# Kernel tuning notes

Hardware: AMD Instinct MI355X
Metric: run time of the kernel (lower is better)

The kernel has to match this reference:

```python
import jax, jax.numpy as jnp
import numpy as np

B, S, D, H = 4, 1024, 1024, 16
HD = D // H


def setup_inputs() -> dict:
    key = jax.random.key(0)
    ks = jax.random.split(key, 8)
    x = jax.random.normal(ks[0], (B, S, D), dtype=jnp.float32)
    attn_bias = jax.random.normal(ks[1], (B, H, S, S), dtype=jnp.float32) * 0.1
    pos_ids = jnp.broadcast_to(jnp.arange(S, dtype=jnp.int32), (B, S))
    lengths = jnp.array([S, S - 64, S - 128, S - 256], dtype=jnp.int32)
    pad_mask = jnp.arange(S)[None, :] >= lengths[:, None]  # True = padded key
    scale = 0.02
    Wq = jax.random.normal(ks[2], (D, D), dtype=jnp.float32) * scale
    Wk = jax.random.normal(ks[3], (D, D), dtype=jnp.float32) * scale
    Wv = jax.random.normal(ks[4], (D, D), dtype=jnp.float32) * scale
    Wo = jax.random.normal(ks[5], (D, D), dtype=jnp.float32) * scale
    bq = jnp.zeros((D,), jnp.float32); bk = jnp.zeros((D,), jnp.float32)
    bv = jnp.zeros((D,), jnp.float32); bo = jnp.zeros((D,), jnp.float32)
    return {"x": x, "attn_bias": attn_bias, "pos_ids": pos_ids, "pad_mask": pad_mask,
            "Wq": Wq, "bq": bq, "Wk": Wk, "bk": bk, "Wv": Wv, "bv": bv, "Wo": Wo, "bo": bo}


def _apply_rotary(q, k, pos_ids):
    # q,k: [B,S,H,HD]; pos_ids: [B,S]
    hd = q.shape[-1]
    inv_freq = 1.0 / (10000.0 ** (jnp.arange(0, hd, 2, dtype=jnp.float32) / hd))
    freqs = pos_ids.astype(jnp.float32)[:, :, None] * inv_freq  # [B,S,HD/2]
    emb = jnp.concatenate([freqs, freqs], axis=-1)[:, :, None, :]  # [B,S,1,HD]
    cos, sin = jnp.cos(emb), jnp.sin(emb)
    def rot_half(t):
        t1, t2 = jnp.split(t, 2, axis=-1)
        return jnp.concatenate([-t2, t1], axis=-1)
    return q * cos + rot_half(q) * sin, k * cos + rot_half(k) * sin


def reference(x, attn_bias, pos_ids, pad_mask, Wq, bq, Wk, bk, Wv, bv, Wo, bo):
    b, s, d = x.shape
    q = (x @ Wq.T + bq).reshape(b, s, H, HD)
    k = (x @ Wk.T + bk).reshape(b, s, H, HD)
    v = (x @ Wv.T + bv).reshape(b, s, H, HD)
    q, k = _apply_rotary(q, k, pos_ids)
    q = q.transpose(0, 2, 1, 3)  # [B,H,S,HD]
    k = k.transpose(0, 2, 1, 3)
    v = v.transpose(0, 2, 1, 3)
    scores = jnp.einsum("bhqd,bhkd->bhqk", q, k) / np.sqrt(HD).astype(np.float32)
    scores = scores + attn_bias
    scores = jnp.where(pad_mask[:, None, None, :], -jnp.inf, scores)
    attn = jax.nn.softmax(scores, axis=-1)  # dropout p=0 -> identity
    out = jnp.einsum("bhqk,bhkd->bqhd", attn, v).reshape(b, s, d)
    metric = k.mean(axis=1)  # mean over heads -> [B,S,HD]
    return out @ Wo.T + bo, metric
```

## Files before the change

kernel.cpp:

```cpp
#include <hip/hip_runtime.h>
#include <hip/hip_bf16.h>

#define SS 1024
#define DD 1024
#define HH 16
#define HDD 64

using f32x4  = __attribute__((ext_vector_type(4))) float;
using bf16x8 = __attribute__((ext_vector_type(8))) __bf16;
using bf16x4 = __attribute__((ext_vector_type(4))) __bf16;

__device__ __forceinline__ void gload_lds16(const void* g, void* l) {
  __builtin_amdgcn_global_load_lds((__attribute__((address_space(1))) void*)g,
                                   (__attribute__((address_space(3))) void*)l, 16, 0, 0);
}

__global__ void convert_kernel(const float4* __restrict__ x, const float4* __restrict__ Wq,
                               const float4* __restrict__ Wk, const float4* __restrict__ Wv,
                               const float4* __restrict__ Wo,
                               bf16x4* __restrict__ xb, bf16x4* __restrict__ wqkvb,
                               bf16x4* __restrict__ wob, float4* __restrict__ metric) {
  int i = blockIdx.x * 256 + threadIdx.x;
  if (blockIdx.x < 256) {
    float4 z = {0.f, 0.f, 0.f, 0.f};
    metric[blockIdx.x * 256 + threadIdx.x] = z;
  }
  float4 v; bf16x4* dst;
  if (i < 1048576)      { v = x[i];              dst = xb + i; }
  else if (i < 1310720) { v = Wq[i - 1048576];   dst = wqkvb + (i - 1048576); }
  else if (i < 1572864) { v = Wk[i - 1310720];   dst = wqkvb + 262144 + (i - 1310720); }
  else if (i < 1835008) { v = Wv[i - 1572864];   dst = wqkvb + 524288 + (i - 1572864); }
  else                  { v = Wo[i - 1835008];   dst = wob + (i - 1835008); }
  bf16x4 o;
  o[0] = (__bf16)v.x; o[1] = (__bf16)v.y; o[2] = (__bf16)v.z; o[3] = (__bf16)v.w;
  *dst = o;
}

template<int EPI>
__global__ __launch_bounds__(256, 2)
void gemm_kernel(const __bf16* __restrict__ A, const __bf16* __restrict__ Bm, int N,
                 const float* __restrict__ b0, const float* __restrict__ b1,
                 const float* __restrict__ b2, const int* __restrict__ pos_ids,
                 __bf16* __restrict__ Qr, __bf16* __restrict__ Kr, __bf16* __restrict__ Vtg,
                 float* __restrict__ metric, float* __restrict__ Cout) {
  __shared__ __align__(16) char smem[17408];
  __bf16* As = (__bf16*)smem;
  __bf16* Bs = (__bf16*)(smem + 8192);
  const int tid = threadIdx.x;
  const int wid = tid >> 6, lane = tid & 63;
  const int g = lane >> 4, cl = lane & 15;
  const int ntn = N >> 7;
  const int bm = blockIdx.x / ntn, bn = blockIdx.x % ntn;
  const int m0 = bm << 7, n0 = bn << 7;
  const int wr = (wid >> 1) << 6, wc = (wid & 1) << 6;

  f32x4 acc[4][4] = {};

  for (int kk = 0; kk < 1024; kk += 32) {
    __syncthreads();
#pragma unroll
    for (int p = 0; p < 2; ++p) {
      int idx = p * 256 + tid;
      gload_lds16(A  + (size_t)(m0 + (idx >> 2)) * 1024 + kk + ((idx & 3) << 3),
                  (char*)As + p * 4096 + wid * 1024);
      gload_lds16(Bm + (size_t)(n0 + (idx >> 2)) * 1024 + kk + ((idx & 3) << 3),
                  (char*)Bs + p * 4096 + wid * 1024);
    }
    __syncthreads();
    bf16x8 fa[4], fb[4];
#pragma unroll
    for (int i = 0; i < 4; ++i)
      fa[i] = *(const bf16x8*)(As + (wr + i * 16 + cl) * 32 + g * 8);
#pragma unroll
    for (int j = 0; j < 4; ++j)
      fb[j] = *(const bf16x8*)(Bs + (wc + j * 16 + cl) * 32 + g * 8);
#pragma unroll
    for (int i = 0; i < 4; ++i)
#pragma unroll
      for (int j = 0; j < 4; ++j)
        acc[i][j] = __builtin_amdgcn_mfma_f32_16x16x32_bf16(fa[i], fb[j], acc[i][j], 0, 0, 0);
  }

  if constexpr (EPI == 1) {
#pragma unroll
    for (int j = 0; j < 4; ++j) {
      int col = n0 + wc + j * 16 + cl;
      float bv = b0[col];
#pragma unroll
      for (int i = 0; i < 4; ++i)
#pragma unroll
        for (int r = 0; r < 4; ++r) {
          int row = m0 + wr + i * 16 + g * 4 + r;
          Cout[(size_t)row * 1024 + col] = acc[i][j][r] + bv;
        }
    }
  } else if (n0 >= 2048) {
    __bf16* vt_s = (__bf16*)smem;
    const int b_ = m0 >> 10, s0 = m0 & 1023;
    const int vbase = n0 - 2048;
#pragma unroll
    for (int phase = 0; phase < 2; ++phase) {
      __syncthreads();
      if ((wid & 1) == phase) {
#pragma unroll
        for (int j = 0; j < 4; ++j) {
          int d = j * 16 + cl;
          float bv = b2[vbase + wc + d];
#pragma unroll
          for (int i = 0; i < 4; ++i)
#pragma unroll
            for (int r = 0; r < 4; ++r)
              vt_s[d * 136 + wr + i * 16 + g * 4 + r] = (__bf16)(acc[i][j][r] + bv);
        }
      }
      __syncthreads();
      int hh = (vbase >> 6) + phase;
#pragma unroll
      for (int p = 0; p < 4; ++p) {
        int d = p * 16 + (tid >> 4), s8 = (tid & 15) * 8;
        bf16x8 v = *(const bf16x8*)(vt_s + d * 136 + s8);
        *(bf16x8*)(Vtg + ((size_t)(b_ * HH + hh) * HDD + d) * SS + s0 + s8) = v;
      }
    }
  } else {
    const int cb = n0 + wc;
    const int region = cb >> 10;
    const int hcol = (cb & 1023) >> 6;
    const int cir = cb & 1023;
    const float* bias = region == 0 ? b0 : b1;
    __bf16* dst = region == 0 ? Qr : Kr;
    float invf0 = exp2f(-0.4152410118609203f * (float)(cl));
    float invf1 = exp2f(-0.4152410118609203f * (float)(16 + cl));
#pragma unroll
    for (int i = 0; i < 4; ++i) {
#pragma unroll
      for (int r = 0; r < 4; ++r) {
        int row = m0 + wr + i * 16 + g * 4 + r;
        int b_ = row >> 10, s = row & 1023;
        size_t ob = ((size_t)(b_ * HH + hcol) * SS + s) * HDD;
        float pos = (float)pos_ids[row];
#pragma unroll
        for (int j = 0; j < 2; ++j) {
          int dlo = j * 16 + cl;
          float vlo = acc[i][j][r]     + bias[cir + dlo];
          float vhi = acc[i][j + 2][r] + bias[cir + dlo + 32];
          float th = pos * (j == 0 ? invf0 : invf1);
          float sn, cs;
          __sincosf(th, &sn, &cs);
          float olo = vlo * cs - vhi * sn;
          float ohi = vhi * cs + vlo * sn;
          dst[ob + dlo]      = (__bf16)olo;
          dst[ob + dlo + 32] = (__bf16)ohi;
          if (region == 1) {
            atomicAdd(&metric[(size_t)row * HDD + dlo],      olo * 0.0625f);
            atomicAdd(&metric[(size_t)row * HDD + dlo + 32], ohi * 0.0625f);
          }
        }
      }
    }
  }
}

__global__ __launch_bounds__(512, 4)
void attn_kernel(const __bf16* __restrict__ Qr, const __bf16* __restrict__ Kr,
                 const __bf16* __restrict__ Vtg, const float* __restrict__ bias,
                 const int* __restrict__ pad, __bf16* __restrict__ attn_out) {
  __shared__ __align__(16) __bf16 Ks[2][64][64];
  __shared__ __align__(16) __bf16 Vt[2][64][64];
  __shared__ __align__(16) __bf16 Plds[8][16][68];
  const int tid = threadIdx.x;
  const int wid = tid >> 6, lane = tid & 63;
  const int g = lane >> 4, cl = lane & 15;
  const int bh = blockIdx.x & 63, b_ = bh >> 4, h = bh & 15;
  const int q0 = (blockIdx.x >> 6) * 128 + wid * 16;
  const __bf16* Qb = Qr  + ((size_t)bh << 16);
  const __bf16* Kb = Kr  + ((size_t)bh << 16);
  const __bf16* Vb = Vtg + ((size_t)bh << 16);
  const float*  Bb = bias + ((size_t)bh << 20);
  const int* padb = pad + b_ * SS;

  int pm = (lane < 16) ? padb[lane * 64] : 1;
  unsigned long long ball = __ballot(pm == 0);
  const int ntile = __popcll(ball & 0xFFFFull);

  const int l8 = lane >> 3, l7 = lane & 7;
  const int krow = 8 * wid + l8;
  const int kchk = l7 ^ l8;
  const int swz = cl & 7;

  gload_lds16(Kb + (size_t)krow * 64 + kchk * 8, (char*)&Ks[0][8 * wid][0]);
  gload_lds16(Vb + (size_t)krow * SS + kchk * 8, (char*)&Vt[0][8 * wid][0]);
  float breg[4][4];
#pragma unroll
  for (int kt = 0; kt < 4; ++kt)
#pragma unroll
    for (int r = 0; r < 4; ++r)
      breg[kt][r] = Bb[(size_t)(q0 + 4 * g + r) * SS + kt * 16 + cl];

  bf16x8 aq0 = *(const bf16x8*)(Qb + (size_t)(q0 + cl) * 64 + g * 8);
  bf16x8 aq1 = *(const bf16x8*)(Qb + (size_t)(q0 + cl) * 64 + 32 + g * 8);
  bf16x8 onesb;
#pragma unroll
  for (int j = 0; j < 8; ++j) onesb[j] = (__bf16)1.0f;

  f32x4 o[4] = {};
  float m_l[4] = {-1e30f, -1e30f, -1e30f, -1e30f};
  float l_l[4] = {0.f, 0.f, 0.f, 0.f};

  for (int t = 0; t < ntile; ++t) {
    const int buf = t & 1;
    __syncthreads();
    if (t + 1 < ntile) {
      int kk = (t + 1) * 64;
      gload_lds16(Kb + (size_t)(kk + krow) * 64 + kchk * 8, (char*)&Ks[buf ^ 1][8 * wid][0]);
      gload_lds16(Vb + (size_t)krow * SS + kk + kchk * 8,   (char*)&Vt[buf ^ 1][8 * wid][0]);
    }

    f32x4 sc[4];
    __builtin_amdgcn_s_setprio(1);
#pragma unroll
    for (int kt = 0; kt < 4; ++kt) {
      bf16x8 kb0 = *(const bf16x8*)(&Ks[buf][kt * 16 + cl][(g ^ swz) * 8]);
      bf16x8 kb1 = *(const bf16x8*)(&Ks[buf][kt * 16 + cl][((g + 4) ^ swz) * 8]);
      f32x4 z = {0.f, 0.f, 0.f, 0.f};
      z = __builtin_amdgcn_mfma_f32_16x16x32_bf16(aq0, kb0, z, 0, 0, 0);
      sc[kt] = __builtin_amdgcn_mfma_f32_16x16x32_bf16(aq1, kb1, z, 0, 0, 0);
    }
    __builtin_amdgcn_s_setprio(0);

#pragma unroll
    for (int kt = 0; kt < 4; ++kt)
#pragma unroll
      for (int r = 0; r < 4; ++r)
        sc[kt][r] = sc[kt][r] * 0.125f + breg[kt][r];
    if (t + 1 < ntile) {
      int kk = (t + 1) * 64;
#pragma unroll
      for (int kt = 0; kt < 4; ++kt)
#pragma unroll
        for (int r = 0; r < 4; ++r)
          breg[kt][r] = Bb[(size_t)(q0 + 4 * g + r) * SS + kk + kt * 16 + cl];
    }

    float mx[4];
#pragma unroll
    for (int r = 0; r < 4; ++r)
      mx[r] = fmaxf(fmaxf(sc[0][r], sc[1][r]), fmaxf(sc[2][r], sc[3][r]));
#pragma unroll
    for (int d = 1; d < 16; d <<= 1)
#pragma unroll
      for (int r = 0; r < 4; ++r) mx[r] = fmaxf(mx[r], __shfl_xor(mx[r], d, 64));
    bool adv = true;
#pragma unroll
    for (int r = 0; r < 4; ++r) adv = adv && (mx[r] <= m_l[r] + 8.0f);
    if (!__all(adv)) {
#pragma unroll
      for (int r = 0; r < 4; ++r) {
        float nm = fmaxf(m_l[r], mx[r]);
        float s_ = __expf(m_l[r] - nm);
        m_l[r] = nm;
        l_l[r] *= s_;
#pragma unroll
        for (int dj = 0; dj < 4; ++dj) o[dj][r] *= s_;
      }
    }
#pragma unroll
    for (int kt = 0; kt < 4; ++kt)
#pragma unroll
      for (int r = 0; r < 4; ++r) sc[kt][r] = __expf(sc[kt][r] - m_l[r]);

#pragma unroll
    for (int kt = 0; kt < 4; ++kt)
#pragma unroll
      for (int r = 0; r < 4; ++r)
        Plds[wid][g * 4 + r][kt * 16 + cl] = (__bf16)sc[kt][r];
    bf16x8 pa0 = *(const bf16x8*)(&Plds[wid][cl][g * 8]);
    bf16x8 pa1 = *(const bf16x8*)(&Plds[wid][cl][32 + g * 8]);

    __builtin_amdgcn_s_setprio(1);
    f32x4 ls = {0.f, 0.f, 0.f, 0.f};
    ls = __builtin_amdgcn_mfma_f32_16x16x32_bf16(pa0, onesb, ls, 0, 0, 0);
    ls = __builtin_amdgcn_mfma_f32_16x16x32_bf16(pa1, onesb, ls, 0, 0, 0);
#pragma unroll
    for (int dj = 0; dj < 4; ++dj) {
      bf16x8 vb0 = *(const bf16x8*)(&Vt[buf][dj * 16 + cl][(g ^ swz) * 8]);
      bf16x8 vb1 = *(const bf16x8*)(&Vt[buf][dj * 16 + cl][((g + 4) ^ swz) * 8]);
      o[dj] = __builtin_amdgcn_mfma_f32_16x16x32_bf16(pa0, vb0, o[dj], 0, 0, 0);
      o[dj] = __builtin_amdgcn_mfma_f32_16x16x32_bf16(pa1, vb1, o[dj], 0, 0, 0);
    }
    __builtin_amdgcn_s_setprio(0);
#pragma unroll
    for (int r = 0; r < 4; ++r) l_l[r] += ls[r];
  }

#pragma unroll
  for (int dj = 0; dj < 4; ++dj)
#pragma unroll
    for (int r = 0; r < 4; ++r) {
      int qrow = q0 + g * 4 + r;
      attn_out[(size_t)(b_ * SS + qrow) * DD + h * 64 + dj * 16 + cl] =
          (__bf16)(o[dj][r] / l_l[r]);
    }
}

extern "C" void kernel_launch(void* const* d_in, const int* in_sizes, int n_in,
                              void* d_out, int out_size, void* d_ws, size_t ws_size,
                              hipStream_t stream) {
  const float* x  = (const float*)d_in[0];
  const float* ab = (const float*)d_in[1];
  const int* pos  = (const int*)d_in[2];
  const int* pad  = (const int*)d_in[3];
  const float* Wq = (const float*)d_in[4];
  const float* bq = (const float*)d_in[5];
  const float* Wk = (const float*)d_in[6];
  const float* bk = (const float*)d_in[7];
  const float* Wv = (const float*)d_in[8];
  const float* bv = (const float*)d_in[9];
  const float* Wo = (const float*)d_in[10];
  const float* bo = (const float*)d_in[11];
  float* out = (float*)d_out;
  float* metric = out + 4194304;

  char* ws = (char*)d_ws;
  __bf16* Qr   = (__bf16*)(ws);
  __bf16* Kr   = (__bf16*)(ws + 8388608);
  __bf16* Vtg  = (__bf16*)(ws + 16777216);
  __bf16* xb   = (__bf16*)(ws + 25165824);
  __bf16* wqkv = (__bf16*)(ws + 33554432);
  __bf16* wob  = (__bf16*)(ws + 39845888);
  __bf16* ao   = (__bf16*)(ws + 41943040);

  convert_kernel<<<8192, 256, 0, stream>>>((const float4*)x, (const float4*)Wq,
                                           (const float4*)Wk, (const float4*)Wv,
                                           (const float4*)Wo, (bf16x4*)xb,
                                           (bf16x4*)wqkv, (bf16x4*)wob, (float4*)metric);
  gemm_kernel<0><<<768, 256, 0, stream>>>(xb, wqkv, 3072, bq, bk, bv, pos,
                                          Qr, Kr, Vtg, metric, nullptr);
  attn_kernel<<<512, 512, 0, stream>>>(Qr, Kr, Vtg, ab, pad, ao);
  gemm_kernel<1><<<256, 256, 0, stream>>>(ao, wob, 1024, bo, nullptr, nullptr, nullptr,
                                          nullptr, nullptr, nullptr, nullptr, out);
}
```

Measured before the change: 170.7 us.

## Templatize GEMM tile width, swizzle block order, and double-buffer attention bias prefetch

```diff
diff --git a/kernel.cpp b/kernel.cpp
--- a/kernel.cpp
+++ b/kernel.cpp
@@ -36,8 +36,8 @@
   *dst = o;
 }
 
-template<int EPI>
-__global__ __launch_bounds__(256, 2)
+template<int EPI, int TN>
+__global__ __launch_bounds__(256, 3)
 void gemm_kernel(const __bf16* __restrict__ A, const __bf16* __restrict__ Bm, int N,
                  const float* __restrict__ b0, const float* __restrict__ b1,
                  const float* __restrict__ b2, const int* __restrict__ pos_ids,
@@ -46,44 +46,50 @@
   __shared__ __align__(16) char smem[17408];
   __bf16* As = (__bf16*)smem;
   __bf16* Bs = (__bf16*)(smem + 8192);
+  constexpr int NJ = TN / 32;
   const int tid = threadIdx.x;
   const int wid = tid >> 6, lane = tid & 63;
   const int g = lane >> 4, cl = lane & 15;
-  const int ntn = N >> 7;
-  const int bm = blockIdx.x / ntn, bn = blockIdx.x % ntn;
-  const int m0 = bm << 7, n0 = bn << 7;
-  const int wr = (wid >> 1) << 6, wc = (wid & 1) << 6;
-
-  f32x4 acc[4][4] = {};
+  const int ntn = N / TN;
+  const int tile = (blockIdx.x & 7) * ((int)gridDim.x >> 3) + (blockIdx.x >> 3);
+  const int bm = tile / ntn, bn = tile % ntn;
+  const int m0 = bm << 7, n0 = bn * TN;
+  const int wr = (wid >> 1) << 6, wc = (wid & 1) * (TN / 2);
+
+  f32x4 acc[4][NJ] = {};
 
   for (int kk = 0; kk < 1024; kk += 32) {
     __syncthreads();
 #pragma unroll
     for (int p = 0; p < 2; ++p) {
       int idx = p * 256 + tid;
-      gload_lds16(A  + (size_t)(m0 + (idx >> 2)) * 1024 + kk + ((idx & 3) << 3),
+      gload_lds16(A + (size_t)(m0 + (idx >> 2)) * 1024 + kk + ((idx & 3) << 3),
                   (char*)As + p * 4096 + wid * 1024);
+    }
+#pragma unroll
+    for (int p = 0; p < TN / 64; ++p) {
+      int idx = p * 256 + tid;
       gload_lds16(Bm + (size_t)(n0 + (idx >> 2)) * 1024 + kk + ((idx & 3) << 3),
                   (char*)Bs + p * 4096 + wid * 1024);
     }
     __syncthreads();
-    bf16x8 fa[4], fb[4];
+    bf16x8 fa[4], fb[NJ];
 #pragma unroll
     for (int i = 0; i < 4; ++i)
       fa[i] = *(const bf16x8*)(As + (wr + i * 16 + cl) * 32 + g * 8);
 #pragma unroll
-    for (int j = 0; j < 4; ++j)
+    for (int j = 0; j < NJ; ++j)
       fb[j] = *(const bf16x8*)(Bs + (wc + j * 16 + cl) * 32 + g * 8);
 #pragma unroll
     for (int i = 0; i < 4; ++i)
 #pragma unroll
-      for (int j = 0; j < 4; ++j)
+      for (int j = 0; j < NJ; ++j)
         acc[i][j] = __builtin_amdgcn_mfma_f32_16x16x32_bf16(fa[i], fb[j], acc[i][j], 0, 0, 0);
   }
 
   if constexpr (EPI == 1) {
 #pragma unroll
-    for (int j = 0; j < 4; ++j) {
+    for (int j = 0; j < NJ; ++j) {
       int col = n0 + wc + j * 16 + cl;
       float bv = b0[col];
 #pragma unroll
@@ -161,6 +167,71 @@
   }
 }
 
+#define TILE_BODY(T, BUF, BCUR, BNXT)                                              \
+  {                                                                                \
+    __syncthreads();                                                               \
+    if ((T) + 1 < ntile) {                                                         \
+      const int kk = ((T) + 1) * 64;                                               \
+      gload_lds16(Kb + (size_t)(kk + krow) * 64 + kchk * 8,                        \
+                  (char*)&Ks[(BUF) ^ 1][8 * wid][0]);                              \
+      gload_lds16(Vb + (size_t)krow * SS + kk + kchk * 8,                          \
+                  (char*)&Vt[(BUF) ^ 1][8 * wid][0]);                              \
+      _Pragma("unroll") for (int kt = 0; kt < 4; ++kt)                             \
+        _Pragma("unroll") for (int r = 0; r < 4; ++r)                              \
+          BNXT[kt][r] = Bb[(size_t)(q0 + 4 * g + r) * SS + kk + kt * 16 + cl];     \
+    }                                                                              \
+    f32x4 sc[4];                                                                   \
+    __builtin_amdgcn_s_setprio(1);                                                 \
+    _Pragma("unroll") for (int kt = 0; kt < 4; ++kt) {                             \
+      bf16x8 kb0 = *(const bf16x8*)(&Ks[(BUF)][kt * 16 + cl][(g ^ swz) * 8]);      \
+      bf16x8 kb1 = *(const bf16x8*)(&Ks[(BUF)][kt * 16 + cl][((g + 4) ^ swz) * 8]);\
+      f32x4 z = {0.f, 0.f, 0.f, 0.f};                                              \
+      z = __builtin_amdgcn_mfma_f32_16x16x32_bf16(aq0, kb0, z, 0, 0, 0);           \
+      sc[kt] = __builtin_amdgcn_mfma_f32_16x16x32_bf16(aq1, kb1, z, 0, 0, 0);      \
+    }                                                                              \
+    __builtin_amdgcn_s_setprio(0);                                                 \
+    _Pragma("unroll") for (int kt = 0; kt < 4; ++kt)                               \
+      _Pragma("unroll") for (int r = 0; r < 4; ++r)                                \
+        sc[kt][r] = sc[kt][r] * 0.125f + BCUR[kt][r];                              \
+    float mx[4];                                                                   \
+    _Pragma("unroll") for (int r = 0; r < 4; ++r)                                  \
+      mx[r] = fmaxf(fmaxf(sc[0][r], sc[1][r]), fmaxf(sc[2][r], sc[3][r]));         \
+    _Pragma("unroll") for (int d = 1; d < 16; d <<= 1)                             \
+      _Pragma("unroll") for (int r = 0; r < 4; ++r)                                \
+        mx[r] = fmaxf(mx[r], __shfl_xor(mx[r], d, 64));                            \
+    bool adv = true;                                                               \
+    _Pragma("unroll") for (int r = 0; r < 4; ++r)                                  \
+      adv = adv && (mx[r] <= m_l[r] + 8.0f);                                       \
+    if (!__all(adv)) {                                                             \
+      _Pragma("unroll") for (int r = 0; r < 4; ++r) {                              \
+        float nm = fmaxf(m_l[r], mx[r]);                                           \
+        float s_ = __expf(m_l[r] - nm);                                            \
+        m_l[r] = nm; l_l[r] *= s_;                                                 \
+        _Pragma("unroll") for (int dj = 0; dj < 4; ++dj) o[dj][r] *= s_;           \
+      }                                                                            \
+    }                                                                              \
+    _Pragma("unroll") for (int kt = 0; kt < 4; ++kt)                               \
+      _Pragma("unroll") for (int r = 0; r < 4; ++r)                                \
+        sc[kt][r] = __expf(sc[kt][r] - m_l[r]);                                    \
+    _Pragma("unroll") for (int kt = 0; kt < 4; ++kt)                               \
+      _Pragma("unroll") for (int r = 0; r < 4; ++r)                                \
+        Plds[wid][g * 4 + r][kt * 16 + cl] = (__bf16)sc[kt][r];                    \
+    bf16x8 pa0 = *(const bf16x8*)(&Plds[wid][cl][g * 8]);                          \
+    bf16x8 pa1 = *(const bf16x8*)(&Plds[wid][cl][32 + g * 8]);                     \
+    __builtin_amdgcn_s_setprio(1);                                                 \
+    f32x4 ls = {0.f, 0.f, 0.f, 0.f};                                               \
+    ls = __builtin_amdgcn_mfma_f32_16x16x32_bf16(pa0, onesb, ls, 0, 0, 0);         \
+    ls = __builtin_amdgcn_mfma_f32_16x16x32_bf16(pa1, onesb, ls, 0, 0, 0);         \
+    _Pragma("unroll") for (int dj = 0; dj < 4; ++dj) {                             \
+      bf16x8 vb0 = *(const bf16x8*)(&Vt[(BUF)][dj * 16 + cl][(g ^ swz) * 8]);      \
+      bf16x8 vb1 = *(const bf16x8*)(&Vt[(BUF)][dj * 16 + cl][((g + 4) ^ swz) * 8]);\
+      o[dj] = __builtin_amdgcn_mfma_f32_16x16x32_bf16(pa0, vb0, o[dj], 0, 0, 0);   \
+      o[dj] = __builtin_amdgcn_mfma_f32_16x16x32_bf16(pa1, vb1, o[dj], 0, 0, 0);   \
+    }                                                                              \
+    __builtin_amdgcn_s_setprio(0);                                                 \
+    _Pragma("unroll") for (int r = 0; r < 4; ++r) l_l[r] += ls[r];                 \
+  }
+
 __global__ __launch_bounds__(512, 4)
 void attn_kernel(const __bf16* __restrict__ Qr, const __bf16* __restrict__ Kr,
                  const __bf16* __restrict__ Vtg, const float* __restrict__ bias,
@@ -190,12 +261,12 @@
 
   gload_lds16(Kb + (size_t)krow * 64 + kchk * 8, (char*)&Ks[0][8 * wid][0]);
   gload_lds16(Vb + (size_t)krow * SS + kchk * 8, (char*)&Vt[0][8 * wid][0]);
-  float breg[4][4];
+  float bregA[4][4], bregB[4][4];
 #pragma unroll
   for (int kt = 0; kt < 4; ++kt)
 #pragma unroll
     for (int r = 0; r < 4; ++r)
-      breg[kt][r] = Bb[(size_t)(q0 + 4 * g + r) * SS + kt * 16 + cl];
+      bregA[kt][r] = Bb[(size_t)(q0 + 4 * g + r) * SS + kt * 16 + cl];
 
   bf16x8 aq0 = *(const bf16x8*)(Qb + (size_t)(q0 + cl) * 64 + g * 8);
   bf16x8 aq1 = *(const bf16x8*)(Qb + (size_t)(q0 + cl) * 64 + 32 + g * 8);
@@ -207,90 +278,9 @@
   float m_l[4] = {-1e30f, -1e30f, -1e30f, -1e30f};
   float l_l[4] = {0.f, 0.f, 0.f, 0.f};
 
-  for (int t = 0; t < ntile; ++t) {
-    const int buf = t & 1;
-    __syncthreads();
-    if (t + 1 < ntile) {
-      int kk = (t + 1) * 64;
-      gload_lds16(Kb + (size_t)(kk + krow) * 64 + kchk * 8, (char*)&Ks[buf ^ 1][8 * wid][0]);
-      gload_lds16(Vb + (size_t)krow * SS + kk + kchk * 8,   (char*)&Vt[buf ^ 1][8 * wid][0]);
-    }
-
-    f32x4 sc[4];
-    __builtin_amdgcn_s_setprio(1);
-#pragma unroll
-    for (int kt = 0; kt < 4; ++kt) {
-      bf16x8 kb0 = *(const bf16x8*)(&Ks[buf][kt * 16 + cl][(g ^ swz) * 8]);
-      bf16x8 kb1 = *(const bf16x8*)(&Ks[buf][kt * 16 + cl][((g + 4) ^ swz) * 8]);
-      f32x4 z = {0.f, 0.f, 0.f, 0.f};
-      z = __builtin_amdgcn_mfma_f32_16x16x32_bf16(aq0, kb0, z, 0, 0, 0);
-      sc[kt] = __builtin_amdgcn_mfma_f32_16x16x32_bf16(aq1, kb1, z, 0, 0, 0);
-    }
-    __builtin_amdgcn_s_setprio(0);
-
-#pragma unroll
-    for (int kt = 0; kt < 4; ++kt)
-#pragma unroll
-      for (int r = 0; r < 4; ++r)
-        sc[kt][r] = sc[kt][r] * 0.125f + breg[kt][r];
-    if (t + 1 < ntile) {
-      int kk = (t + 1) * 64;
-#pragma unroll
-      for (int kt = 0; kt < 4; ++kt)
-#pragma unroll
-        for (int r = 0; r < 4; ++r)
-          breg[kt][r] = Bb[(size_t)(q0 + 4 * g + r) * SS + kk + kt * 16 + cl];
-    }
-
-    float mx[4];
-#pragma unroll
-    for (int r = 0; r < 4; ++r)
-      mx[r] = fmaxf(fmaxf(sc[0][r], sc[1][r]), fmaxf(sc[2][r], sc[3][r]));
-#pragma unroll
-    for (int d = 1; d < 16; d <<= 1)
-#pragma unroll
-      for (int r = 0; r < 4; ++r) mx[r] = fmaxf(mx[r], __shfl_xor(mx[r], d, 64));
-    bool adv = true;
-#pragma unroll
-    for (int r = 0; r < 4; ++r) adv = adv && (mx[r] <= m_l[r] + 8.0f);
-    if (!__all(adv)) {
-#pragma unroll
-      for (int r = 0; r < 4; ++r) {
-        float nm = fmaxf(m_l[r], mx[r]);
-        float s_ = __expf(m_l[r] - nm);
-        m_l[r] = nm;
-        l_l[r] *= s_;
-#pragma unroll
-        for (int dj = 0; dj < 4; ++dj) o[dj][r] *= s_;
-      }
-    }
-#pragma unroll
-    for (int kt = 0; kt < 4; ++kt)
-#pragma unroll
-      for (int r = 0; r < 4; ++r) sc[kt][r] = __expf(sc[kt][r] - m_l[r]);
-
-#pragma unroll
-    for (int kt = 0; kt < 4; ++kt)
-#pragma unroll
-      for (int r = 0; r < 4; ++r)
-        Plds[wid][g * 4 + r][kt * 16 + cl] = (__bf16)sc[kt][r];
-    bf16x8 pa0 = *(const bf16x8*)(&Plds[wid][cl][g * 8]);
-    bf16x8 pa1 = *(const bf16x8*)(&Plds[wid][cl][32 + g * 8]);
-
-    __builtin_amdgcn_s_setprio(1);
-    f32x4 ls = {0.f, 0.f, 0.f, 0.f};
-    ls = __builtin_amdgcn_mfma_f32_16x16x32_bf16(pa0, onesb, ls, 0, 0, 0);
-    ls = __builtin_amdgcn_mfma_f32_16x16x32_bf16(pa1, onesb, ls, 0, 0, 0);
-#pragma unroll
-    for (int dj = 0; dj < 4; ++dj) {
-      bf16x8 vb0 = *(const bf16x8*)(&Vt[buf][dj * 16 + cl][(g ^ swz) * 8]);
-      bf16x8 vb1 = *(const bf16x8*)(&Vt[buf][dj * 16 + cl][((g + 4) ^ swz) * 8]);
-      o[dj] = __builtin_amdgcn_mfma_f32_16x16x32_bf16(pa0, vb0, o[dj], 0, 0, 0);
-      o[dj] = __builtin_amdgcn_mfma_f32_16x16x32_bf16(pa1, vb1, o[dj], 0, 0, 0);
-    }
-    __builtin_amdgcn_s_setprio(0);
-#pragma unroll
-    for (int r = 0; r < 4; ++r) l_l[r] += ls[r];
+  for (int t = 0; t < ntile; t += 2) {
+    TILE_BODY(t, 0, bregA, bregB);
+    if (t + 1 < ntile) TILE_BODY(t + 1, 1, bregB, bregA);
   }
 
 #pragma unroll
@@ -334,9 +324,9 @@
                                            (const float4*)Wk, (const float4*)Wv,
                                            (const float4*)Wo, (bf16x4*)xb,
                                            (bf16x4*)wqkv, (bf16x4*)wob, (float4*)metric);
-  gemm_kernel<0><<<768, 256, 0, stream>>>(xb, wqkv, 3072, bq, bk, bv, pos,
-                                          Qr, Kr, Vtg, metric, nullptr);
+  gemm_kernel<0, 128><<<768, 256, 0, stream>>>(xb, wqkv, 3072, bq, bk, bv, pos,
+                                               Qr, Kr, Vtg, metric, nullptr);
   attn_kernel<<<512, 512, 0, stream>>>(Qr, Kr, Vtg, ab, pad, ao);
-  gemm_kernel<1><<<256, 256, 0, stream>>>(ao, wob, 1024, bo, nullptr, nullptr, nullptr,
-                                          nullptr, nullptr, nullptr, nullptr, out);
-}
+  gemm_kernel<1, 64><<<512, 256, 0, stream>>>(ao, wob, 1024, bo, nullptr, nullptr, nullptr,
+                                              nullptr, nullptr, nullptr, nullptr, out);
+}
```

Result: no change. 173.6 us (+1.7%).
